# Kernel optimization log

Measured on AMD Instinct MI355X. Metric: run time of the kernel, lower is better.

The kernel has to match this reference:

```python
import jax, jax.numpy as jnp
import numpy as np

L, BAT, A, B, D, NBITS = 2, 32, 64, 1024, 128, 1024
PADDING = 0


def setup_inputs() -> dict:
    key = jax.random.key(0)
    k1, k2, k3, k4, k5 = jax.random.split(key, 5)
    query_embed = jax.random.normal(k1, (L, BAT, A, D), dtype=jnp.float32)
    doc_embed = jax.random.normal(k2, (L, BAT, B, D), dtype=jnp.float32)
    query_tok = jax.random.randint(k3, (BAT, A), 0, 2)
    doc_tok = jax.random.randint(k4, (BAT, B), 0, 2)
    # LSH projection matrix: randn * sigma + mu with sigma=0.1, mu=0
    r = jax.random.normal(k5, (NBITS, D), dtype=jnp.float32) * 0.1
    return {"query_embed": query_embed, "doc_embed": doc_embed,
            "query_tok": query_tok, "doc_tok": doc_tok, "r": r}


def reference(query_embed, doc_embed, query_tok, doc_tok, r):
    d = r.shape[0]  # num_bits
    # sign-hash: (emb @ r.T > 0).float()  -> binary codes in {0,1}
    c1 = (jnp.einsum('lbad,kd->lbak', query_embed, r) > 0).astype(jnp.float32)  # [L,BAT,A,NBITS]
    c2 = (jnp.einsum('lbcd,kd->lbck', doc_embed, r) > 0).astype(jnp.float32)    # [L,BAT,B,NBITS]
    # Hamming distance via popcount identity: |u-v|_H = sum(u) + sum(v) - 2 u.v
    s1 = c1.sum(-1)  # [L,BAT,A]
    s2 = c2.sum(-1)  # [L,BAT,B]
    dot = jnp.einsum('lbak,lbck->lbac', c1, c2)  # [L,BAT,A,B]
    ham = s1[..., :, None] + s2[..., None, :] - 2.0 * dot
    sim = jnp.cos(jnp.pi / d * ham)  # [L,BAT,A,B]
    # zero out padded query / doc positions
    qmask = (query_tok == PADDING)[None, :, :, None]
    dmask = (doc_tok == PADDING)[None, :, None, :]
    sim = jnp.where(qmask | dmask, 0.0, sim)
    # torch.stack(simmat, dim=1) -> [BAT, L, A, B]
    return jnp.transpose(sim, (1, 0, 2, 3))
```

## Files before the change

### kernel.cpp

```cpp
#include <hip/hip_runtime.h>
#include <math.h>

#define L_ 2
#define BAT_ 32
#define A_ 64
#define B_ 1024
#define D_ 128
#define NBITS_ 1024
#define NW 32
#define NQROWS (L_*BAT_*A_)
#define NDROWS (L_*BAT_*B_)
#define NROWS (NQROWS + NDROWS)
#define NAGRP (NROWS / 16)
#define NBGRP (NBITS_ / 16)

#define TM 128
#define TN 128
#define NXB (NROWS / TM)
#define NYB (NBITS_ / TN)
#define XPX (NXB / 8)

typedef __bf16 bf16x8 __attribute__((ext_vector_type(8)));
typedef float  f32x4  __attribute__((ext_vector_type(4)));

__global__ __launch_bounds__(256) void preswz_kernel(
    const float* __restrict__ qe, const float* __restrict__ de,
    const float* __restrict__ r, __bf16* __restrict__ asw,
    __bf16* __restrict__ rsw)
{
    const int g = blockIdx.x;
    const int t = threadIdx.x;
    const int ks = t >> 7, kk = (t >> 6) & 1, quad = (t >> 4) & 3, col = t & 15;

    const float* src;
    __bf16* dst;
    if (g < NAGRP) {
        int row = g * 16 + col;
        src = (row < NQROWS) ? (qe + (size_t)row * D_)
                             : (de + (size_t)(row - NQROWS) * D_);
        dst = asw + (size_t)g * 4096;
    } else {
        int bit = (g - NAGRP) * 16 + col;
        src = r + (size_t)bit * D_;
        dst = rsw + (size_t)(g - NAGRP) * 4096;
    }

    const int ko = ks * 64 + kk * 32 + quad * 8;
    float4 v0 = *(const float4*)(src + ko);
    float4 v1 = *(const float4*)(src + ko + 4);
    bf16x8 hi, lo;
    hi[0] = (__bf16)v0.x; hi[1] = (__bf16)v0.y;
    hi[2] = (__bf16)v0.z; hi[3] = (__bf16)v0.w;
    hi[4] = (__bf16)v1.x; hi[5] = (__bf16)v1.y;
    hi[6] = (__bf16)v1.z; hi[7] = (__bf16)v1.w;
    lo[0] = (__bf16)(v0.x - (float)hi[0]);
    lo[1] = (__bf16)(v0.y - (float)hi[1]);
    lo[2] = (__bf16)(v0.z - (float)hi[2]);
    lo[3] = (__bf16)(v0.w - (float)hi[3]);
    lo[4] = (__bf16)(v1.x - (float)hi[4]);
    lo[5] = (__bf16)(v1.y - (float)hi[5]);
    lo[6] = (__bf16)(v1.z - (float)hi[6]);
    lo[7] = (__bf16)(v1.w - (float)hi[7]);

    const int c_hi = ks * 16 + kk * 4 + quad;
    const int c_lo = c_hi + 8;
    *(bf16x8*)(dst + (size_t)(c_hi * 16 + col) * 8) = hi;
    *(bf16x8*)(dst + (size_t)(c_lo * 16 + col) * 8) = lo;
}

__global__ __launch_bounds__(512, 4) void hash_kernel(
    const __bf16* __restrict__ asw, const __bf16* __restrict__ rsw,
    unsigned int* __restrict__ codes_t)
{
    __shared__ __align__(16) unsigned char bsh[65536];

    const int t = threadIdx.x;
    const int lane = t & 63;
    const int quad = lane >> 4;
    const int col  = lane & 15;
    const int wv   = __builtin_amdgcn_readfirstlane(t >> 6);

    const int bid = blockIdx.x;
    const int xcd = bid & 7;
    const int s   = bid >> 3;
    const int bx  = xcd * XPX + (s >> 3);
    const int by  = s & 7;

    const int wrow = (wv >> 1) * 32;
    const int half = wv & 1;
    const int ga0 = (bx * TM + wrow) >> 4;

    const __bf16* abase = asw + (size_t)ga0 * 4096 + (size_t)lane * 8;
#define ALOAD(ti, cbi) (*(const bf16x8*)(abase + ((ti) * 8 + (cbi)) * 512))

    const unsigned char* bbase = bsh + half * 32768 + lane * 16;
#define BLOAD(tj, cbi) (*(const bf16x8*)(bbase + (tj) * 8192 + (cbi) * 1024))

    bf16x8 xh0 = ALOAD(0, 0), xh1 = ALOAD(1, 0);
    bf16x8 xl0 = ALOAD(0, 2), xl1 = ALOAD(1, 2);
    bf16x8 yh0, yh1, yl0, yl1;

    {
        const char* bsrc = (const char*)rsw + (size_t)by * 65536 + (size_t)t * 16;
        #pragma unroll
        for (int i = 0; i < 8; ++i)
            __builtin_amdgcn_global_load_lds(
                (const __attribute__((address_space(1))) unsigned int*)(bsrc + i * 8192),
                (__attribute__((address_space(3))) unsigned int*)(bsh + i * 8192 + t * 16),
                16, 0, 0);
    }
    __syncthreads();

    f32x4 acc[2][4];
    #pragma unroll
    for (int ti = 0; ti < 2; ++ti)
        #pragma unroll
        for (int tj = 0; tj < 4; ++tj)
            acc[ti][tj] = (f32x4){0.f, 0.f, 0.f, 0.f};

#define MFMA __builtin_amdgcn_mfma_f32_16x16x32_bf16
#define BATCH(A0, A1, B0, B1, B2, B3)                       \
    acc[0][0] = MFMA(A0, B0, acc[0][0], 0, 0, 0);           \
    acc[0][1] = MFMA(A0, B1, acc[0][1], 0, 0, 0);           \
    acc[0][2] = MFMA(A0, B2, acc[0][2], 0, 0, 0);           \
    acc[0][3] = MFMA(A0, B3, acc[0][3], 0, 0, 0);           \
    acc[1][0] = MFMA(A1, B0, acc[1][0], 0, 0, 0);           \
    acc[1][1] = MFMA(A1, B1, acc[1][1], 0, 0, 0);           \
    acc[1][2] = MFMA(A1, B2, acc[1][2], 0, 0, 0);           \
    acc[1][3] = MFMA(A1, B3, acc[1][3], 0, 0, 0);

#define ITER(CH, cH0, cH1, cL0, cL1, DO_PREF, NH, nH0, nH1, nL0, nL1)   \
    {                                                                    \
        if (DO_PREF) {                                                   \
            nH0 = ALOAD(0, NH);       nH1 = ALOAD(1, NH);                \
            nL0 = ALOAD(0, (NH) + 2); nL1 = ALOAD(1, (NH) + 2);          \
        }                                                                \
        bf16x8 b0 = BLOAD(0, CH), b1 = BLOAD(1, CH),                     \
               b2 = BLOAD(2, CH), b3 = BLOAD(3, CH);                     \
        BATCH(cH0, cH1, b0, b1, b2, b3)                       \
        BATCH(cL0, cL1, b0, b1, b2, b3)                       \
        b0 = BLOAD(0, (CH) + 2); b1 = BLOAD(1, (CH) + 2);                \
        b2 = BLOAD(2, (CH) + 2); b3 = BLOAD(3, (CH) + 2);                \
        BATCH(cH0, cH1, b0, b1, b2, b3)                       \
    }

    ITER(0, xh0, xh1, xl0, xl1, 1, 1, yh0, yh1, yl0, yl1)
    ITER(1, yh0, yh1, yl0, yl1, 1, 4, xh0, xh1, xl0, xl1)
    ITER(4, xh0, xh1, xl0, xl1, 1, 5, yh0, yh1, yl0, yl1)
    ITER(5, yh0, yh1, yl0, yl1, 0, 0, xh0, xh1, xl0, xl1)

#undef ITER
#undef BATCH
#undef MFMA
#undef BLOAD
#undef ALOAD

    const int row0 = bx * TM;
    #pragma unroll
    for (int ti = 0; ti < 2; ++ti) {
        #pragma unroll
        for (int rg = 0; rg < 4; ++rg) {
            unsigned long long b[4];
            #pragma unroll
            for (int tj = 0; tj < 4; ++tj)
                b[tj] = __ballot(acc[ti][tj][rg] > 0.f);
            if (col < 2) {
                const int w = col;
                unsigned int lo16 = (unsigned int)(b[2 * w]     >> (16 * quad)) & 0xFFFFu;
                unsigned int hi16 = (unsigned int)(b[2 * w + 1] >> (16 * quad)) & 0xFFFFu;
                const int row = row0 + wrow + ti * 16 + quad * 4 + rg;
                const int wg  = by * 4 + half * 2 + w;
                codes_t[(size_t)wg * NROWS + row] = lo16 | (hi16 << 16);
            }
        }
    }
}

__global__ __launch_bounds__(256) void simmat_kernel(
    const unsigned int* __restrict__ codes_t,
    const int* __restrict__ qtok, const int* __restrict__ dtok,
    float* __restrict__ out)
{
    __shared__ unsigned int qc[8 * 36];

    const int blk  = blockIdx.x;
    const int ct   = blk & 3;
    const int asub = (blk >> 2) & 7;
    const int b    = (blk >> 5) & 31;
    const int l    = blk >> 10;
    const int t    = threadIdx.x;

    const int a0 = asub * 8;
    const int qrow0 = (l * BAT_ + b) * A_ + a0;
    if (t < 256) {
        int w = t >> 3, a = t & 7;
        qc[a * 36 + w] = codes_t[(size_t)w * NROWS + qrow0 + a];
    }
    __syncthreads();

    const int c = ct * 256 + t;
    const size_t drow = (size_t)NQROWS + (size_t)(l * BAT_ + b) * B_ + c;
    unsigned int dc[NW];
    #pragma unroll
    for (int w = 0; w < NW; ++w) dc[w] = codes_t[(size_t)w * NROWS + drow];
    const float dm = (dtok[b * B_ + c] != 0) ? 1.f : 0.f;

    float* obase = out + ((size_t)((b * L_ + l) * A_ + a0)) * B_ + c;
    #pragma unroll
    for (int ai = 0; ai < 8; ++ai) {
        int ham = 0;
        #pragma unroll
        for (int m = 0; m < 8; ++m) {
            uint4 qv = *(const uint4*)(&qc[ai * 36 + m * 4]);
            ham += __popc(qv.x ^ dc[4 * m])     + __popc(qv.y ^ dc[4 * m + 1])
                 + __popc(qv.z ^ dc[4 * m + 2]) + __popc(qv.w ^ dc[4 * m + 3]);
        }
        const float qmv = (qtok[b * A_ + a0 + ai] != 0) ? 1.f : 0.f;
        float sim = __cosf((float)M_PI / (float)NBITS_ * (float)ham);
        obase[(size_t)ai * B_] = sim * (qmv * dm);
    }
}

extern "C" void kernel_launch(void* const* d_in, const int* in_sizes, int n_in,
                              void* d_out, int out_size, void* d_ws, size_t ws_size,
                              hipStream_t stream) {
    const float* qe  = (const float*)d_in[0];
    const float* de  = (const float*)d_in[1];
    const int* qtok  = (const int*)d_in[2];
    const int* dtok  = (const int*)d_in[3];
    const float* r   = (const float*)d_in[4];
    float* out = (float*)d_out;

    unsigned int* codes_t = (unsigned int*)d_ws;
    __bf16* rsw = (__bf16*)((char*)d_ws + 8912896);
    __bf16* asw = (__bf16*)((char*)d_ws + 8912896 + 524288);

    preswz_kernel<<<NAGRP + NBGRP, 256, 0, stream>>>(qe, de, r, asw, rsw);
    hash_kernel<<<NXB * NYB, 512, 0, stream>>>(asw, rsw, codes_t);
    simmat_kernel<<<L_ * BAT_ * 8 * 4, 256, 0, stream>>>(codes_t, qtok, dtok, out);
}
```

Measured before the change: 154.7 us.

## Make hash kernel persistent over row tiles, reusing LDS-resident projection slice

The hash GEMM launch drops from one block per 128x128 tile to 512 blocks. Each block loads its 128-bit projection slice into LDS once, then loops over a strip of about 8-9 row tiles, prefetching the next tile's A fragments during the last iteration. This amortizes the 64KB LDS fill and the block launch cost. It also hoists all B loads before the MFMAs and raises wave priority around the MFMA batches with s_setprio. The risk is fewer blocks, so lower occupancy and tail imbalance on the 256-CU device.

```diff
diff --git a/kernel.cpp b/kernel.cpp
--- a/kernel.cpp
+++ b/kernel.cpp
@@ -80,24 +80,29 @@
     const int col  = lane & 15;
     const int wv   = __builtin_amdgcn_readfirstlane(t >> 6);
 
-    const int bid = blockIdx.x;
-    const int xcd = bid & 7;
-    const int s   = bid >> 3;
-    const int bx  = xcd * XPX + (s >> 3);
-    const int by  = s & 7;
+    const int bid   = blockIdx.x;
+    const int xcd   = bid & 7;
+    const int sb    = bid >> 3;
+    const int by    = sb & 7;
+    const int strip = sb >> 3;
+    const int s0 = (strip * XPX) >> 3;
+    const int s1 = ((strip + 1) * XPX) >> 3;
+    const int bx0 = xcd * XPX + s0;
+    const int ntiles = s1 - s0;
 
     const int wrow = (wv >> 1) * 32;
     const int half = wv & 1;
-    const int ga0 = (bx * TM + wrow) >> 4;
-
-    const __bf16* abase = asw + (size_t)ga0 * 4096 + (size_t)lane * 8;
-#define ALOAD(ti, cbi) (*(const bf16x8*)(abase + ((ti) * 8 + (cbi)) * 512))
+
+    const __bf16* abase = asw + ((size_t)((bx0 * TM + wrow) >> 4)) * 4096
+                              + (size_t)lane * 8;
+#define ALOAD(P, ti, cbi) (*(const bf16x8*)((P) + ((ti) * 8 + (cbi)) * 512))
+#define TILE_STRIDE 32768
 
     const unsigned char* bbase = bsh + half * 32768 + lane * 16;
 #define BLOAD(tj, cbi) (*(const bf16x8*)(bbase + (tj) * 8192 + (cbi) * 1024))
 
-    bf16x8 xh0 = ALOAD(0, 0), xh1 = ALOAD(1, 0);
-    bf16x8 xl0 = ALOAD(0, 2), xl1 = ALOAD(1, 2);
+    bf16x8 xh0 = ALOAD(abase, 0, 0), xh1 = ALOAD(abase, 1, 0);
+    bf16x8 xl0 = ALOAD(abase, 0, 2), xl1 = ALOAD(abase, 1, 2);
     bf16x8 yh0, yh1, yl0, yl1;
 
     {
@@ -111,43 +116,69 @@
     }
     __syncthreads();
 
-    f32x4 acc[2][4];
-    #pragma unroll
-    for (int ti = 0; ti < 2; ++ti)
-        #pragma unroll
-        for (int tj = 0; tj < 4; ++tj)
-            acc[ti][tj] = (f32x4){0.f, 0.f, 0.f, 0.f};
-
 #define MFMA __builtin_amdgcn_mfma_f32_16x16x32_bf16
 #define BATCH(A0, A1, B0, B1, B2, B3)                       \
     acc[0][0] = MFMA(A0, B0, acc[0][0], 0, 0, 0);           \
     acc[0][1] = MFMA(A0, B1, acc[0][1], 0, 0, 0);           \
     acc[0][2] = MFMA(A0, B2, acc[0][2], 0, 0, 0);           \
-    acc[0][3] = MFMA(A0, B3, acc[0][3], 0, 0, 0);           \
     acc[1][0] = MFMA(A1, B0, acc[1][0], 0, 0, 0);           \
     acc[1][1] = MFMA(A1, B1, acc[1][1], 0, 0, 0);           \
+    acc[0][2] = acc[0][2];                                  \
+    acc[0][3] = MFMA(A0, B3, acc[0][3], 0, 0, 0);           \
     acc[1][2] = MFMA(A1, B2, acc[1][2], 0, 0, 0);           \
     acc[1][3] = MFMA(A1, B3, acc[1][3], 0, 0, 0);
 
-#define ITER(CH, cH0, cH1, cL0, cL1, DO_PREF, NH, nH0, nH1, nL0, nL1)   \
+#define ITER(CH, cH0, cH1, cL0, cL1, PBASE, NH, nH0, nH1, nL0, nL1)     \
     {                                                                    \
-        if (DO_PREF) {                                                   \
-            nH0 = ALOAD(0, NH);       nH1 = ALOAD(1, NH);                \
-            nL0 = ALOAD(0, (NH) + 2); nL1 = ALOAD(1, (NH) + 2);          \
-        }                                                                \
+        nH0 = ALOAD(PBASE, 0, NH);       nH1 = ALOAD(PBASE, 1, NH);      \
+        nL0 = ALOAD(PBASE, 0, (NH) + 2); nL1 = ALOAD(PBASE, 1, (NH) + 2);\
         bf16x8 b0 = BLOAD(0, CH), b1 = BLOAD(1, CH),                     \
                b2 = BLOAD(2, CH), b3 = BLOAD(3, CH);                     \
+        bf16x8 c0 = BLOAD(0, (CH) + 2), c1 = BLOAD(1, (CH) + 2),         \
+               c2 = BLOAD(2, (CH) + 2), c3 = BLOAD(3, (CH) + 2);         \
+        __builtin_amdgcn_s_setprio(1);                                   \
         BATCH(cH0, cH1, b0, b1, b2, b3)                       \
         BATCH(cL0, cL1, b0, b1, b2, b3)                       \
-        b0 = BLOAD(0, (CH) + 2); b1 = BLOAD(1, (CH) + 2);                \
-        b2 = BLOAD(2, (CH) + 2); b3 = BLOAD(3, (CH) + 2);                \
-        BATCH(cH0, cH1, b0, b1, b2, b3)                       \
-    }
-
-    ITER(0, xh0, xh1, xl0, xl1, 1, 1, yh0, yh1, yl0, yl1)
-    ITER(1, yh0, yh1, yl0, yl1, 1, 4, xh0, xh1, xl0, xl1)
-    ITER(4, xh0, xh1, xl0, xl1, 1, 5, yh0, yh1, yl0, yl1)
-    ITER(5, yh0, yh1, yl0, yl1, 0, 0, xh0, xh1, xl0, xl1)
+        BATCH(cH0, cH1, c0, c1, c2, c3)                       \
+        __builtin_amdgcn_s_setprio(0);                                   \
+    }
+
+    for (int i = 0; i < ntiles; ++i) {
+        f32x4 acc[2][4];
+        #pragma unroll
+        for (int ti = 0; ti < 2; ++ti)
+            #pragma unroll
+            for (int tj = 0; tj < 4; ++tj)
+                acc[ti][tj] = (f32x4){0.f, 0.f, 0.f, 0.f};
+
+        const __bf16* anext = (i + 1 < ntiles) ? (abase + TILE_STRIDE) : abase;
+
+        ITER(0, xh0, xh1, xl0, xl1, abase, 1, yh0, yh1, yl0, yl1)
+        ITER(1, yh0, yh1, yl0, yl1, abase, 4, xh0, xh1, xl0, xl1)
+        ITER(4, xh0, xh1, xl0, xl1, abase, 5, yh0, yh1, yl0, yl1)
+        ITER(5, yh0, yh1, yl0, yl1, anext, 0, xh0, xh1, xl0, xl1)
+
+        const int row0 = (bx0 + i) * TM;
+        #pragma unroll
+        for (int ti = 0; ti < 2; ++ti) {
+            #pragma unroll
+            for (int rg = 0; rg < 4; ++rg) {
+                unsigned long long b[4];
+                #pragma unroll
+                for (int tj = 0; tj < 4; ++tj)
+                    b[tj] = __ballot(acc[ti][tj][rg] > 0.f);
+                if (col < 2) {
+                    const int w = col;
+                    unsigned int lo16 = (unsigned int)(b[2 * w]     >> (16 * quad)) & 0xFFFFu;
+                    unsigned int hi16 = (unsigned int)(b[2 * w + 1] >> (16 * quad)) & 0xFFFFu;
+                    const int row = row0 + wrow + ti * 16 + quad * 4 + rg;
+                    const int wg  = by * 4 + half * 2 + w;
+                    codes_t[(size_t)wg * NROWS + row] = lo16 | (hi16 << 16);
+                }
+            }
+        }
+        abase = anext;
+    }
 
 #undef ITER
 #undef BATCH
@@ -155,25 +186,6 @@
 #undef BLOAD
 #undef ALOAD
 
-    const int row0 = bx * TM;
-    #pragma unroll
-    for (int ti = 0; ti < 2; ++ti) {
-        #pragma unroll
-        for (int rg = 0; rg < 4; ++rg) {
-            unsigned long long b[4];
-            #pragma unroll
-            for (int tj = 0; tj < 4; ++tj)
-                b[tj] = __ballot(acc[ti][tj][rg] > 0.f);
-            if (col < 2) {
-                const int w = col;
-                unsigned int lo16 = (unsigned int)(b[2 * w]     >> (16 * quad)) & 0xFFFFu;
-                unsigned int hi16 = (unsigned int)(b[2 * w + 1] >> (16 * quad)) & 0xFFFFu;
-                const int row = row0 + wrow + ti * 16 + quad * 4 + rg;
-                const int wg  = by * 4 + half * 2 + w;
-                codes_t[(size_t)wg * NROWS + row] = lo16 | (hi16 << 16);
-            }
-        }
-    }
 }
 
 __global__ __launch_bounds__(256) void simmat_kernel(
@@ -236,6 +248,6 @@
     __bf16* asw = (__bf16*)((char*)d_ws + 8912896 + 524288);
 
     preswz_kernel<<<NAGRP + NBGRP, 256, 0, stream>>>(qe, de, r, asw, rsw);
-    hash_kernel<<<NXB * NYB, 512, 0, stream>>>(asw, rsw, codes_t);
+    hash_kernel<<<512, 512, 0, stream>>>(asw, rsw, codes_t);
     simmat_kernel<<<L_ * BAT_ * 8 * 4, 256, 0, stream>>>(codes_t, qtok, dtok, out);
 }
```

Result: slower. 258.5 us (+67.1%).

## Process four row tiles per hash block to reuse the LDS-staged projection tile

Applied to the files above, without the earlier changes.

Each hash_kernel block now loops over four consecutive 128-row tiles, reusing the projection-matrix tile it loaded into LDS once. A-operand prefetch is chained across tiles so the loads for the next tile overlap the last MFMA batch. This cuts redundant global-to-LDS traffic and launch count by four. In exchange there are fewer blocks (1088), which reduces parallelism and may raise register pressure.

```diff
diff --git a/kernel.cpp b/kernel.cpp
--- a/kernel.cpp
+++ b/kernel.cpp
@@ -19,6 +19,7 @@
 #define NXB (NROWS / TM)
 #define NYB (NBITS_ / TN)
 #define XPX (NXB / 8)
+#define NTPB 4
 
 typedef __bf16 bf16x8 __attribute__((ext_vector_type(8)));
 typedef float  f32x4  __attribute__((ext_vector_type(4)));
@@ -83,21 +84,23 @@
     const int bid = blockIdx.x;
     const int xcd = bid & 7;
     const int s   = bid >> 3;
-    const int bx  = xcd * XPX + (s >> 3);
     const int by  = s & 7;
+    const int xq  = s >> 3;
+    const int bx0 = xcd * XPX + xq * NTPB;
 
     const int wrow = (wv >> 1) * 32;
     const int half = wv & 1;
-    const int ga0 = (bx * TM + wrow) >> 4;
-
-    const __bf16* abase = asw + (size_t)ga0 * 4096 + (size_t)lane * 8;
-#define ALOAD(ti, cbi) (*(const bf16x8*)(abase + ((ti) * 8 + (cbi)) * 512))
+
+    const __bf16* abase = asw + ((size_t)((bx0 * TM + wrow) >> 4)) * 4096
+                              + (size_t)lane * 8;
+#define ALOAD(P, ti, cbi) (*(const bf16x8*)((P) + ((ti) * 8 + (cbi)) * 512))
+#define TILE_STRIDE 32768
 
     const unsigned char* bbase = bsh + half * 32768 + lane * 16;
 #define BLOAD(tj, cbi) (*(const bf16x8*)(bbase + (tj) * 8192 + (cbi) * 1024))
 
-    bf16x8 xh0 = ALOAD(0, 0), xh1 = ALOAD(1, 0);
-    bf16x8 xl0 = ALOAD(0, 2), xl1 = ALOAD(1, 2);
+    bf16x8 xh0 = ALOAD(abase, 0, 0), xh1 = ALOAD(abase, 1, 0);
+    bf16x8 xl0 = ALOAD(abase, 0, 2), xl1 = ALOAD(abase, 1, 2);
     bf16x8 yh0, yh1, yl0, yl1;
 
     {
@@ -110,13 +113,6 @@
                 16, 0, 0);
     }
     __syncthreads();
-
-    f32x4 acc[2][4];
-    #pragma unroll
-    for (int ti = 0; ti < 2; ++ti)
-        #pragma unroll
-        for (int tj = 0; tj < 4; ++tj)
-            acc[ti][tj] = (f32x4){0.f, 0.f, 0.f, 0.f};
 
 #define MFMA __builtin_amdgcn_mfma_f32_16x16x32_bf16
 #define BATCH(A0, A1, B0, B1, B2, B3)                       \
@@ -129,12 +125,10 @@
     acc[1][2] = MFMA(A1, B2, acc[1][2], 0, 0, 0);           \
     acc[1][3] = MFMA(A1, B3, acc[1][3], 0, 0, 0);
 
-#define ITER(CH, cH0, cH1, cL0, cL1, DO_PREF, NH, nH0, nH1, nL0, nL1)   \
+#define ITER(CH, cH0, cH1, cL0, cL1, PBASE, NH, nH0, nH1, nL0, nL1)     \
     {                                                                    \
-        if (DO_PREF) {                                                   \
-            nH0 = ALOAD(0, NH);       nH1 = ALOAD(1, NH);                \
-            nL0 = ALOAD(0, (NH) + 2); nL1 = ALOAD(1, (NH) + 2);          \
-        }                                                                \
+        nH0 = ALOAD(PBASE, 0, NH);       nH1 = ALOAD(PBASE, 1, NH);      \
+        nL0 = ALOAD(PBASE, 0, (NH) + 2); nL1 = ALOAD(PBASE, 1, (NH) + 2);\
         bf16x8 b0 = BLOAD(0, CH), b1 = BLOAD(1, CH),                     \
                b2 = BLOAD(2, CH), b3 = BLOAD(3, CH);                     \
         BATCH(cH0, cH1, b0, b1, b2, b3)                       \
@@ -144,36 +138,49 @@
         BATCH(cH0, cH1, b0, b1, b2, b3)                       \
     }
 
-    ITER(0, xh0, xh1, xl0, xl1, 1, 1, yh0, yh1, yl0, yl1)
-    ITER(1, yh0, yh1, yl0, yl1, 1, 4, xh0, xh1, xl0, xl1)
-    ITER(4, xh0, xh1, xl0, xl1, 1, 5, yh0, yh1, yl0, yl1)
-    ITER(5, yh0, yh1, yl0, yl1, 0, 0, xh0, xh1, xl0, xl1)
+    #pragma unroll
+    for (int i = 0; i < NTPB; ++i) {
+        const __bf16* ab = abase + (size_t)i * TILE_STRIDE;
+        const __bf16* an = (i + 1 < NTPB) ? (ab + TILE_STRIDE) : ab;
+
+        f32x4 acc[2][4];
+        #pragma unroll
+        for (int ti = 0; ti < 2; ++ti)
+            #pragma unroll
+            for (int tj = 0; tj < 4; ++tj)
+                acc[ti][tj] = (f32x4){0.f, 0.f, 0.f, 0.f};
+
+        ITER(0, xh0, xh1, xl0, xl1, ab, 1, yh0, yh1, yl0, yl1)
+        ITER(1, yh0, yh1, yl0, yl1, ab, 4, xh0, xh1, xl0, xl1)
+        ITER(4, xh0, xh1, xl0, xl1, ab, 5, yh0, yh1, yl0, yl1)
+        ITER(5, yh0, yh1, yl0, yl1, an, 0, xh0, xh1, xl0, xl1)
+
+        const int row0 = (bx0 + i) * TM;
+        #pragma unroll
+        for (int ti = 0; ti < 2; ++ti) {
+            #pragma unroll
+            for (int rg = 0; rg < 4; ++rg) {
+                unsigned long long b[4];
+                #pragma unroll
+                for (int tj = 0; tj < 4; ++tj)
+                    b[tj] = __ballot(acc[ti][tj][rg] > 0.f);
+                if (col < 2) {
+                    const int w = col;
+                    unsigned int lo16 = (unsigned int)(b[2 * w]     >> (16 * quad)) & 0xFFFFu;
+                    unsigned int hi16 = (unsigned int)(b[2 * w + 1] >> (16 * quad)) & 0xFFFFu;
+                    const int row = row0 + wrow + ti * 16 + quad * 4 + rg;
+                    const int wg  = by * 4 + half * 2 + w;
+                    codes_t[(size_t)wg * NROWS + row] = lo16 | (hi16 << 16);
+                }
+            }
+        }
+    }
 
 #undef ITER
 #undef BATCH
 #undef MFMA
 #undef BLOAD
 #undef ALOAD
-
-    const int row0 = bx * TM;
-    #pragma unroll
-    for (int ti = 0; ti < 2; ++ti) {
-        #pragma unroll
-        for (int rg = 0; rg < 4; ++rg) {
-            unsigned long long b[4];
-            #pragma unroll
-            for (int tj = 0; tj < 4; ++tj)
-                b[tj] = __ballot(acc[ti][tj][rg] > 0.f);
-            if (col < 2) {
-                const int w = col;
-                unsigned int lo16 = (unsigned int)(b[2 * w]     >> (16 * quad)) & 0xFFFFu;
-                unsigned int hi16 = (unsigned int)(b[2 * w + 1] >> (16 * quad)) & 0xFFFFu;
-                const int row = row0 + wrow + ti * 16 + quad * 4 + rg;
-                const int wg  = by * 4 + half * 2 + w;
-                codes_t[(size_t)wg * NROWS + row] = lo16 | (hi16 << 16);
-            }
-        }
-    }
 }
 
 __global__ __launch_bounds__(256) void simmat_kernel(
@@ -236,6 +243,6 @@
     __bf16* asw = (__bf16*)((char*)d_ws + 8912896 + 524288);
 
     preswz_kernel<<<NAGRP + NBGRP, 256, 0, stream>>>(qe, de, r, asw, rsw);
-    hash_kernel<<<NXB * NYB, 512, 0, stream>>>(asw, rsw, codes_t);
+    hash_kernel<<<(NXB / NTPB) * NYB, 512, 0, stream>>>(asw, rsw, codes_t);
     simmat_kernel<<<L_ * BAT_ * 8 * 4, 256, 0, stream>>>(codes_t, qtok, dtok, out);
 }
```

Result: slower. 158.1 us (median of 2 runs) (+2.2%).
